# Kernel optimization log

Hardware: AMD Instinct MI355X
Metric: run time of the kernel (lower is better)

The kernel has to match this reference:

```python
import jax, jax.numpy as jnp
import numpy as np

N_NODES = 100000
N_EDGES = 1600000
D_IN = 128
D_H = 128
N_LAYERS = 3
N_OUT = 10
N_GRAPHS = 64


def setup_inputs() -> dict:
    key = jax.random.key(0)
    ks = jax.random.split(key, 12)
    glorot = lambda k, fi, fo: jax.random.normal(k, (fi, fo), jnp.float32) * np.sqrt(2.0 / (fi + fo))
    return {
        "x": jax.random.normal(ks[0], (N_NODES, D_IN), jnp.float32),
        "edge_index": jax.random.randint(ks[1], (2, N_EDGES), 0, N_NODES, jnp.int64 if jax.config.jax_enable_x64 else jnp.int32),
        "batch": jnp.sort(jax.random.randint(ks[2], (N_NODES,), 0, N_GRAPHS)),
        "target_size": N_GRAPHS,
        "W1": glorot(ks[3], D_IN, D_H), "b1": jnp.zeros((D_H,), jnp.float32),
        "W2": glorot(ks[4], D_H, D_H), "b2": jnp.zeros((D_H,), jnp.float32),
        "W3": glorot(ks[5], D_H, D_H), "b3": jnp.zeros((D_H,), jnp.float32),
        "lin1_w": glorot(ks[6], N_LAYERS * D_H, D_H), "lin1_b": jnp.zeros((D_H,), jnp.float32),
        "lin2_w": glorot(ks[7], D_H, N_OUT), "lin2_b": jnp.zeros((N_OUT,), jnp.float32),
    }


def _gcn_conv(x, src, dst, norm, W, b, n_nodes):
    # PyG GCNConv: h = X W; out[dst] += norm * h[src]; out += b
    h = x @ W
    msg = h[src] * norm[:, None]            # [E+N, D_H] gathered messages
    out = jax.ops.segment_sum(msg, dst, num_segments=n_nodes)
    return out + b


def reference(x, edge_index, batch, target_size, W1, b1, W2, b2, W3, b3,
              lin1_w, lin1_b, lin2_w, lin2_b):
    n = x.shape[0]
    loops = jnp.arange(n, dtype=edge_index.dtype)
    src = jnp.concatenate([edge_index[0], loops])   # add self-loops (PyG default)
    dst = jnp.concatenate([edge_index[1], loops])
    deg = jax.ops.segment_sum(jnp.ones_like(src, dtype=x.dtype), dst, num_segments=n)
    dinv = jnp.where(deg > 0, jax.lax.rsqrt(deg), 0.0)
    norm = dinv[src] * dinv[dst]                    # symmetric normalization

    h1 = jax.nn.relu(_gcn_conv(x, src, dst, norm, W1, b1, n))
    h2 = jax.nn.relu(_gcn_conv(h1, src, dst, norm, W2, b2, n))
    h3 = jax.nn.relu(_gcn_conv(h2, src, dst, norm, W3, b3, n))
    h = jnp.concatenate([h1, h2, h3], axis=-1)      # JumpingKnowledge 'cat' -> [N, 3*D_H]

    # global_mean_pool over graphs
    counts = jax.ops.segment_sum(jnp.ones((n,), x.dtype), batch, num_segments=target_size)
    pooled = jax.ops.segment_sum(h, batch, num_segments=target_size)
    pooled = pooled / jnp.maximum(counts, 1.0)[:, None]

    g = jax.nn.relu(pooled @ lin1_w + lin1_b)       # dropout is identity at inference
    logits = g @ lin2_w + lin2_b
    return jax.nn.log_softmax(logits, axis=-1)
```

## Files before the change

kernel.cpp:

```cpp
#include <hip/hip_runtime.h>

#define NN 100000
#define NE 1600000
#define DH 128
#define NG 64

#define NBUCKU 98
#define EPB 4096
#define NBLK_BIN 391
#define CAP 20480

#define LDH 136

typedef __attribute__((ext_vector_type(2))) _Float16 half2v;
typedef __attribute__((ext_vector_type(4))) _Float16 half4;
typedef __attribute__((ext_vector_type(8))) _Float16 half8;
typedef __attribute__((ext_vector_type(4))) float f32x4;

__device__ inline unsigned int enc8(_Float16 h) {
  unsigned short b = __builtin_bit_cast(unsigned short, h);
  unsigned short r = (unsigned short)(b + 0x7F + ((b >> 8) & 1));
  return (unsigned int)(r >> 8);
}
__device__ inline half2v d02(unsigned int u) {
  return __builtin_bit_cast(half2v, (u << 8) & 0xFF00FF00u);
}
__device__ inline half2v d13(unsigned int u) {
  return __builtin_bit_cast(half2v, u & 0xFF00FF00u);
}


__global__ __launch_bounds__(256) void k_build(const int* __restrict__ esrc,
                                               const int* __restrict__ edst,
                                               const int* __restrict__ batch,
                                               const float* __restrict__ W0,
                                               const float* __restrict__ W1,
                                               const float* __restrict__ W2,
                                               int* __restrict__ bucketCursor,
                                               unsigned int* __restrict__ pairs,
                                               int* __restrict__ startg,
                                               _Float16* __restrict__ Wt) {
  int b = blockIdx.x, t = threadIdx.x;
  int gtid = b * 256 + t;

  if (gtid < 3 * DH * DH) {
    int l = gtid >> 14;
    int rem = gtid & 16383;
    int n = rem >> 7, k = rem & 127;
    const float* W = (l == 0) ? W0 : (l == 1) ? W1 : W2;
    Wt[(size_t)l * DH * DH + n * DH + k] = (_Float16)W[k * DH + n];
  }
  if (gtid < NN) {
    int bat = batch[gtid];
    int prev = (gtid == 0) ? -1 : batch[gtid - 1];
    for (int g = prev + 1; g <= bat; ++g) startg[g] = gtid;
    if (gtid == NN - 1)
      for (int g = bat + 1; g <= NG; ++g) startg[g] = NN;
  }

  __shared__ int h[NBUCKU];
  __shared__ int cur[NBUCKU];
  if (t < NBUCKU) h[t] = 0;
  __syncthreads();
  int base = b * EPB;
#pragma unroll
  for (int i = 0; i < EPB / 256; ++i) {
    int e = base + i * 256 + t;
    if (e < NE) atomicAdd(&h[edst[e] >> 10], 1);
  }
  __syncthreads();
  if (t < NBUCKU) {
    int rel = atomicAdd(&bucketCursor[t], h[t]);
    cur[t] = t * CAP + rel;
  }
  __syncthreads();
#pragma unroll
  for (int i = 0; i < EPB / 256; ++i) {
    int e = base + i * 256 + t;
    if (e < NE) {
      int d = edst[e];
      int q = atomicAdd(&cur[d >> 10], 1);
      pairs[q] = ((unsigned int)esrc[e] << 10) | (unsigned int)(d & 1023);
    }
  }
}


__global__ __launch_bounds__(256) void k_finalize(const unsigned int* __restrict__ pairs,
                                                  const int* __restrict__ bucketCursor,
                                                  int* __restrict__ offA,
                                                  int* __restrict__ offB,
                                                  float* __restrict__ dinv,
                                                  int* __restrict__ csr_src) {
  __shared__ int cnt[1024];
  __shared__ int tsum[256];
  int b = blockIdx.x, t = threadIdx.x;
  int nodeBase = b << 10;
  for (int i = t; i < 1024; i += 256) cnt[i] = 0;
  __syncthreads();
  int pStart = b * CAP;
  int pEnd = pStart + bucketCursor[b];
  for (int p = pStart + t; p < pEnd; p += 256)
    atomicAdd(&cnt[pairs[p] & 1023], 1);
  __syncthreads();
  int c0 = cnt[t * 4], c1 = cnt[t * 4 + 1], c2 = cnt[t * 4 + 2], c3 = cnt[t * 4 + 3];
  tsum[t] = c0 + c1 + c2 + c3;
  __syncthreads();
  for (int off = 1; off < 256; off <<= 1) {
    int v = (t >= off) ? tsum[t - off] : 0;
    __syncthreads();
    tsum[t] += v;
    __syncthreads();
  }
  int basep = pStart + ((t > 0) ? tsum[t - 1] : 0);
  int e0 = basep, e1 = basep + c0, e2 = e1 + c1, e3 = e2 + c2;
  __syncthreads();
  cnt[t * 4] = e0; cnt[t * 4 + 1] = e1; cnt[t * 4 + 2] = e2; cnt[t * 4 + 3] = e3;
  int g = nodeBase + t * 4;
  if (g < NN)     { offA[g] = e0;     offB[g] = e1;      dinv[g] = rsqrtf((float)c0 + 1.f); }
  if (g + 1 < NN) { offA[g + 1] = e1; offB[g + 1] = e2;  dinv[g + 1] = rsqrtf((float)c1 + 1.f); }
  if (g + 2 < NN) { offA[g + 2] = e2; offB[g + 2] = e3;  dinv[g + 2] = rsqrtf((float)c2 + 1.f); }
  if (g + 3 < NN) { offA[g + 3] = e3; offB[g + 3] = e3 + c3; dinv[g + 3] = rsqrtf((float)c3 + 1.f); }
  __syncthreads();
  for (int p = pStart + t; p < pEnd; p += 256) {
    unsigned int pr = pairs[p];
    int pos = atomicAdd(&cnt[pr & 1023], 1);
    csr_src[pos] = (int)(pr >> 10);
  }
}


template <bool F32IN>
__global__ __launch_bounds__(256) void k_gemm(const void* __restrict__ Ap,
                                              const _Float16* __restrict__ Wt,
                                              const float* __restrict__ dinv,
                                              unsigned char* __restrict__ Out8) {
  __shared__ _Float16 Wl[128 * LDH];
  int tid = threadIdx.x;
  int rowBase = blockIdx.x * 128;

#pragma unroll
  for (int i = 0; i < 8; ++i) {
    int chunk = tid + i * 256;
    int r = chunk >> 4, c = (chunk & 15) * 8;
    *(half8*)&Wl[r * LDH + c] = *(const half8*)(Wt + r * DH + c);
  }

  int wv = tid >> 6;
  int lane = tid & 63;
  int n16 = lane & 15;
  int quad = lane >> 4;

  int r0 = rowBase + wv * 32 + n16;
  int r1 = r0 + 16;

  half8 af[2][4];
  if (F32IN) {
    const float* A = (const float*)Ap;
#pragma unroll
    for (int kk = 0; kk < 4; ++kk) {
      half8 z = {};
      if (r0 < NN) {
        float4 lo = *(const float4*)(A + (size_t)r0 * DH + quad * 8 + kk * 32);
        float4 hi = *(const float4*)(A + (size_t)r0 * DH + quad * 8 + kk * 32 + 4);
        z = (half8){(_Float16)lo.x, (_Float16)lo.y, (_Float16)lo.z, (_Float16)lo.w,
                    (_Float16)hi.x, (_Float16)hi.y, (_Float16)hi.z, (_Float16)hi.w};
      }
      af[0][kk] = z;
      half8 z1 = {};
      if (r1 < NN) {
        float4 lo = *(const float4*)(A + (size_t)r1 * DH + quad * 8 + kk * 32);
        float4 hi = *(const float4*)(A + (size_t)r1 * DH + quad * 8 + kk * 32 + 4);
        z1 = (half8){(_Float16)lo.x, (_Float16)lo.y, (_Float16)lo.z, (_Float16)lo.w,
                     (_Float16)hi.x, (_Float16)hi.y, (_Float16)hi.z, (_Float16)hi.w};
      }
      af[1][kk] = z1;
    }
  } else {
    const _Float16* A = (const _Float16*)Ap;
#pragma unroll
    for (int kk = 0; kk < 4; ++kk) {
      half8 z = {};
      if (r0 < NN) z = *(const half8*)(A + (size_t)r0 * DH + quad * 8 + kk * 32);
      af[0][kk] = z;
      half8 z1 = {};
      if (r1 < NN) z1 = *(const half8*)(A + (size_t)r1 * DH + quad * 8 + kk * 32);
      af[1][kk] = z1;
    }
  }
  __syncthreads();

  f32x4 acc[2][8];
#pragma unroll
  for (int mt = 0; mt < 2; ++mt)
#pragma unroll
    for (int ct = 0; ct < 8; ++ct) acc[mt][ct] = (f32x4){0.f, 0.f, 0.f, 0.f};

  const _Float16* bp = &Wl[n16 * LDH + quad * 8];
#pragma unroll
  for (int kk = 0; kk < 4; ++kk) {
#pragma unroll
    for (int ct = 0; ct < 8; ++ct) {
      half8 bf = *(const half8*)(bp + (size_t)ct * 16 * LDH + kk * 32);
      acc[0][ct] = __builtin_amdgcn_mfma_f32_16x16x32_f16(af[0][kk], bf, acc[0][ct], 0, 0, 0);
      acc[1][ct] = __builtin_amdgcn_mfma_f32_16x16x32_f16(af[1][kk], bf, acc[1][ct], 0, 0, 0);
    }
  }

  float dv[2][4];
#pragma unroll
  for (int mt = 0; mt < 2; ++mt)
#pragma unroll
    for (int r = 0; r < 4; ++r) {
      int gr = rowBase + wv * 32 + mt * 16 + quad * 4 + r;
      dv[mt][r] = (gr < NN) ? dinv[gr] : 0.f;
    }

  __syncthreads();
#pragma unroll
  for (int mt = 0; mt < 2; ++mt)
#pragma unroll
    for (int ct = 0; ct < 8; ++ct)
#pragma unroll
      for (int r = 0; r < 4; ++r)
        Wl[(wv * 32 + mt * 16 + quad * 4 + r) * LDH + ct * 16 + n16] =
            (_Float16)(acc[mt][ct][r] * dv[mt][r]);
  __syncthreads();

#pragma unroll
  for (int i = 0; i < 8; ++i) {
    int chunk = tid + i * 256;
    int r = chunk >> 4, c = (chunk & 15) * 8;
    int gr = rowBase + r;
    if (gr < NN) {
      half8 v = *(const half8*)&Wl[r * LDH + c];
      unsigned int lo = enc8(v[0]) | (enc8(v[1]) << 8) | (enc8(v[2]) << 16) | (enc8(v[3]) << 24);
      unsigned int hi = enc8(v[4]) | (enc8(v[5]) << 8) | (enc8(v[6]) << 16) | (enc8(v[7]) << 24);
      uint2 st = {lo, hi};
      *(uint2*)(Out8 + (size_t)gr * DH + c) = st;
    }
  }
}


__global__ __launch_bounds__(512) void k_fused(const unsigned char* __restrict__ hs8_in,
                                               const int* __restrict__ csr_src,
                                               const int* __restrict__ offA,
                                               const int* __restrict__ offB,
                                               const float* __restrict__ dinv,
                                               const float* __restrict__ bias,
                                               const int* __restrict__ batch,
                                               const int* __restrict__ startg,
                                               float* __restrict__ pooled,
                                               int colOff,
                                               const _Float16* __restrict__ Wt,
                                               unsigned char* __restrict__ hs8_out) {
  __shared__ _Float16 Hl[64 * LDH];
  __shared__ _Float16 Wl[128 * LDH];
  int tid = threadIdx.x;
  int n0 = blockIdx.x * 64;

#pragma unroll
  for (int i = 0; i < 4; ++i) {
    int chunk = tid + i * 512;
    int r = chunk >> 4, c = (chunk & 15) * 8;
    *(half8*)&Wl[r * LDH + c] = *(const half8*)(Wt + r * DH + c);
  }

  int nd = tid >> 3;
  int part = tid & 7;
  int n = n0 + nd;
  bool valid = (n < NN);

  half2v acc[8];
#pragma unroll
  for (int i = 0; i < 8; ++i) acc[i] = (half2v){(_Float16)0, (_Float16)0};

  if (valid) {
    const unsigned char* bp = hs8_in + part * 16;
    uint4 us = *(const uint4*)(bp + (size_t)n * DH);
    acc[0] += d02(us.x); acc[1] += d13(us.x);
    acc[2] += d02(us.y); acc[3] += d13(us.y);
    acc[4] += d02(us.z); acc[5] += d13(us.z);
    acc[6] += d02(us.w); acc[7] += d13(us.w);
    int s = offA[n], e = offB[n];
    int p = s;
    for (; p + 3 < e; p += 4) {
      int s0 = csr_src[p], s1 = csr_src[p + 1], s2 = csr_src[p + 2], s3 = csr_src[p + 3];
      uint4 u0 = *(const uint4*)(bp + (size_t)s0 * DH);
      uint4 u1 = *(const uint4*)(bp + (size_t)s1 * DH);
      uint4 u2 = *(const uint4*)(bp + (size_t)s2 * DH);
      uint4 u3 = *(const uint4*)(bp + (size_t)s3 * DH);
      acc[0] += d02(u0.x); acc[1] += d13(u0.x); acc[2] += d02(u0.y); acc[3] += d13(u0.y);
      acc[4] += d02(u0.z); acc[5] += d13(u0.z); acc[6] += d02(u0.w); acc[7] += d13(u0.w);
      acc[0] += d02(u1.x); acc[1] += d13(u1.x); acc[2] += d02(u1.y); acc[3] += d13(u1.y);
      acc[4] += d02(u1.z); acc[5] += d13(u1.z); acc[6] += d02(u1.w); acc[7] += d13(u1.w);
      acc[0] += d02(u2.x); acc[1] += d13(u2.x); acc[2] += d02(u2.y); acc[3] += d13(u2.y);
      acc[4] += d02(u2.z); acc[5] += d13(u2.z); acc[6] += d02(u2.w); acc[7] += d13(u2.w);
      acc[0] += d02(u3.x); acc[1] += d13(u3.x); acc[2] += d02(u3.y); acc[3] += d13(u3.y);
      acc[4] += d02(u3.z); acc[5] += d13(u3.z); acc[6] += d02(u3.w); acc[7] += d13(u3.w);
    }
    for (; p < e; ++p) {
      int s0 = csr_src[p];
      uint4 u0 = *(const uint4*)(bp + (size_t)s0 * DH);
      acc[0] += d02(u0.x); acc[1] += d13(u0.x); acc[2] += d02(u0.y); acc[3] += d13(u0.y);
      acc[4] += d02(u0.z); acc[5] += d13(u0.z); acc[6] += d02(u0.w); acc[7] += d13(u0.w);
    }
  }

  float dv = valid ? dinv[n] : 0.f;
#pragma unroll
  for (int w = 0; w < 4; ++w) {
    int dim = part * 16 + w * 4;
    float4 b4 = *(const float4*)(bias + dim);
    float h0 = valid ? fmaxf(fmaf((float)acc[2 * w][0], dv, b4.x), 0.f) : 0.f;
    float h1 = valid ? fmaxf(fmaf((float)acc[2 * w + 1][0], dv, b4.y), 0.f) : 0.f;
    float h2 = valid ? fmaxf(fmaf((float)acc[2 * w][1], dv, b4.z), 0.f) : 0.f;
    float h3 = valid ? fmaxf(fmaf((float)acc[2 * w + 1][1], dv, b4.w), 0.f) : 0.f;
    half4 hh = {(_Float16)h0, (_Float16)h1, (_Float16)h2, (_Float16)h3};
    *(half4*)&Hl[nd * LDH + dim] = hh;
  }
  __syncthreads();

  if (tid < DH) {
    int nEnd = (n0 + 64 < NN) ? n0 + 64 : NN;
    int gF = batch[n0];
    int gL = batch[nEnd - 1];
    for (int g = gF; g <= gL; ++g) {
      int rs = (startg[g] > n0) ? startg[g] : n0;
      int re = (startg[g + 1] < nEnd) ? startg[g + 1] : nEnd;
      if (re > rs) {
        float sum = 0.f;
        for (int r2 = rs; r2 < re; ++r2) sum += (float)Hl[(r2 - n0) * LDH + tid];
        atomicAdd(&pooled[g * (3 * DH) + colOff + tid], sum);
      }
    }
  }

  int wv = tid >> 6;
  int lane = tid & 63;
  int n16 = lane & 15;
  int quad = lane >> 4;
  int m16 = wv >> 1;
  int ctB = (wv & 1) * 4;

  f32x4 acc2[4];
#pragma unroll
  for (int ct = 0; ct < 4; ++ct) acc2[ct] = (f32x4){0.f, 0.f, 0.f, 0.f};

  const _Float16* ap = &Hl[(m16 * 16 + n16) * LDH + quad * 8];
#pragma unroll
  for (int kk = 0; kk < 4; ++kk) {
    half8 af = *(const half8*)(ap + kk * 32);
#pragma unroll
    for (int ct = 0; ct < 4; ++ct) {
      half8 bf = *(const half8*)&Wl[((ctB + ct) * 16 + n16) * LDH + quad * 8 + kk * 32];
      acc2[ct] = __builtin_amdgcn_mfma_f32_16x16x32_f16(af, bf, acc2[ct], 0, 0, 0);
    }
  }

  float dvo[4];
#pragma unroll
  for (int rr = 0; rr < 4; ++rr) {
    int gr = n0 + m16 * 16 + quad * 4 + rr;
    dvo[rr] = (gr < NN) ? dinv[gr] : 0.f;
  }

  __syncthreads();
#pragma unroll
  for (int ct = 0; ct < 4; ++ct)
#pragma unroll
    for (int rr = 0; rr < 4; ++rr)
      Hl[(m16 * 16 + quad * 4 + rr) * LDH + (ctB + ct) * 16 + n16] =
          (_Float16)(acc2[ct][rr] * dvo[rr]);
  __syncthreads();

#pragma unroll
  for (int i = 0; i < 2; ++i) {
    int chunk = tid + i * 512;
    int r = chunk >> 4, c = (chunk & 15) * 8;
    int gr = n0 + r;
    if (gr < NN) {
      half8 v = *(const half8*)&Hl[r * LDH + c];
      unsigned int lo = enc8(v[0]) | (enc8(v[1]) << 8) | (enc8(v[2]) << 16) | (enc8(v[3]) << 24);
      unsigned int hi = enc8(v[4]) | (enc8(v[5]) << 8) | (enc8(v[6]) << 16) | (enc8(v[7]) << 24);
      uint2 st = {lo, hi};
      *(uint2*)(hs8_out + (size_t)gr * DH + c) = st;
    }
  }
}


__global__ __launch_bounds__(256) void k_aggregate(const unsigned char* __restrict__ hs8,
                                                   const int* __restrict__ csr_src,
                                                   const int* __restrict__ offA,
                                                   const int* __restrict__ offB,
                                                   const float* __restrict__ dinv,
                                                   const float* __restrict__ bias,
                                                   const int* __restrict__ batch,
                                                   float* __restrict__ pooled,
                                                   int colOff) {
  __shared__ float stage[8][DH];
  int tid = threadIdx.x;
  int gid = blockIdx.x * 256 + tid;
  int node = gid >> 5;
  int sub = tid >> 5;
  int lane4 = (gid & 31) * 4;
  int s = offA[node];
  int e = offB[node];

  unsigned int us = *(const unsigned int*)(hs8 + (size_t)node * DH + lane4);
  half2v aE0 = d02(us), aE1 = d13(us);
  half2v aO0 = {(_Float16)0, (_Float16)0}, aO1 = {(_Float16)0, (_Float16)0};

  int p = s;
  for (; p + 3 < e; p += 4) {
    int s0 = csr_src[p];
    int s1 = csr_src[p + 1];
    int s2 = csr_src[p + 2];
    int s3 = csr_src[p + 3];
    unsigned int u0 = *(const unsigned int*)(hs8 + (size_t)s0 * DH + lane4);
    unsigned int u1 = *(const unsigned int*)(hs8 + (size_t)s1 * DH + lane4);
    unsigned int u2 = *(const unsigned int*)(hs8 + (size_t)s2 * DH + lane4);
    unsigned int u3 = *(const unsigned int*)(hs8 + (size_t)s3 * DH + lane4);
    aE0 += d02(u0); aE1 += d13(u0);
    aO0 += d02(u1); aO1 += d13(u1);
    aE0 += d02(u2); aE1 += d13(u2);
    aO0 += d02(u3); aO1 += d13(u3);
  }
  for (; p < e; ++p) {
    int s0 = csr_src[p];
    unsigned int u0 = *(const unsigned int*)(hs8 + (size_t)s0 * DH + lane4);
    aE0 += d02(u0); aE1 += d13(u0);
  }

  float ax = (float)aE0[0] + (float)aO0[0];
  float ay = (float)aE1[0] + (float)aO1[0];
  float az = (float)aE0[1] + (float)aO0[1];
  float aw = (float)aE1[1] + (float)aO1[1];

  float dv = dinv[node];
  float4 b4 = *(const float4*)(bias + lane4);
  float4 r;
  r.x = fmaxf(fmaf(ax, dv, b4.x), 0.f);
  r.y = fmaxf(fmaf(ay, dv, b4.y), 0.f);
  r.z = fmaxf(fmaf(az, dv, b4.z), 0.f);
  r.w = fmaxf(fmaf(aw, dv, b4.w), 0.f);

  int nodeFirst = blockIdx.x * 8;
  int gFirst = batch[nodeFirst];
  int gLast = batch[nodeFirst + 7];
  if (gFirst == gLast) {
    *(float4*)&stage[sub][lane4] = r;
    __syncthreads();
    if (tid < DH) {
      float ssum = 0.f;
#pragma unroll
      for (int w = 0; w < 8; ++w) ssum += stage[w][tid];
      atomicAdd(&pooled[gFirst * (3 * DH) + colOff + tid], ssum);
    }
  } else {
    int g = batch[node];
    float* pp = &pooled[g * (3 * DH) + colOff + lane4];
    atomicAdd(pp + 0, r.x);
    atomicAdd(pp + 1, r.y);
    atomicAdd(pp + 2, r.z);
    atomicAdd(pp + 3, r.w);
  }
}


__global__ __launch_bounds__(128) void k_head(const float* __restrict__ pooled,
                                              const int* __restrict__ startg,
                                              const float* __restrict__ l1w,
                                              const float* __restrict__ l1b,
                                              const float* __restrict__ l2w,
                                              const float* __restrict__ l2b,
                                              float* __restrict__ out) {
  __shared__ float pr[3 * DH];
  __shared__ float grow[DH];
  __shared__ float lg[16];
  int g = blockIdx.x, t = threadIdx.x;
  float cnt = (float)(startg[g + 1] - startg[g]);
  float inv = 1.0f / fmaxf(cnt, 1.0f);
  for (int k = t; k < 3 * DH; k += 128) pr[k] = pooled[g * (3 * DH) + k] * inv;
  __syncthreads();
  float acc = l1b[t];
  for (int k = 0; k < 3 * DH; ++k) acc = fmaf(pr[k], l1w[k * DH + t], acc);
  grow[t] = fmaxf(acc, 0.f);
  __syncthreads();
  if (t < 10) {
    float a = l2b[t];
    for (int k = 0; k < DH; ++k) a = fmaf(grow[k], l2w[k * 10 + t], a);
    lg[t] = a;
  }
  __syncthreads();
  if (t < 10) {
    float m = lg[0];
    for (int i = 1; i < 10; ++i) m = fmaxf(m, lg[i]);
    float sum = 0.f;
    for (int i = 0; i < 10; ++i) sum += expf(lg[i] - m);
    out[g * 10 + t] = lg[t] - m - logf(sum);
  }
}


extern "C" void kernel_launch(void* const* d_in, const int* in_sizes, int n_in,
                              void* d_out, int out_size, void* d_ws, size_t ws_size,
                              hipStream_t stream) {
  const float* x = (const float*)d_in[0];
  const int* ei = (const int*)d_in[1];
  const int* esrc = ei;
  const int* edst = ei + NE;
  const int* batch = (const int*)d_in[2];
  const float* W0 = (const float*)d_in[4];
  const float* W1 = (const float*)d_in[6];
  const float* W2 = (const float*)d_in[8];
  const float* B[3] = {(const float*)d_in[5], (const float*)d_in[7], (const float*)d_in[9]};
  const float* l1w = (const float*)d_in[10];
  const float* l1b = (const float*)d_in[11];
  const float* l2w = (const float*)d_in[12];
  const float* l2b = (const float*)d_in[13];
  float* out = (float*)d_out;

  char* ws = (char*)d_ws;
  size_t off = 0;
  auto alloc = [&](size_t bytes) {
    char* p = ws + off;
    off = (off + bytes + 255) & ~(size_t)255;
    return p;
  };
  float* pooled = (float*)alloc((size_t)NG * 3 * DH * 4);
  int* bucketCursor = (int*)alloc(NBUCKU * 4);
  size_t msBytes = (size_t)NG * 3 * DH * 4 + 512;

  int* offA = (int*)alloc((size_t)NN * 4);
  int* offB = (int*)alloc((size_t)NN * 4);
  float* dinv = (float*)alloc((size_t)NN * 4);
  int* startg = (int*)alloc((NG + 1) * 4);
  _Float16* Wt = (_Float16*)alloc((size_t)3 * DH * DH * 2);
  unsigned char* hs8A = (unsigned char*)alloc((size_t)NN * DH);
  unsigned char* hs8B = (unsigned char*)alloc((size_t)NN * DH);
  unsigned int* pairs = (unsigned int*)alloc((size_t)NBUCKU * CAP * 4);
  int* csr_src = (int*)alloc((size_t)NBUCKU * CAP * 4);

  hipMemsetAsync(pooled, 0, msBytes, stream);

  k_build<<<NBLK_BIN, 256, 0, stream>>>(esrc, edst, batch, W0, W1, W2,
                                        bucketCursor, pairs, startg, Wt);
  k_finalize<<<NBUCKU, 256, 0, stream>>>(pairs, bucketCursor, offA, offB, dinv, csr_src);

  k_gemm<true><<<(NN + 127) / 128, 256, 0, stream>>>((const void*)x, Wt, dinv, hs8A);

  int nFusedBlk = (NN + 63) / 64;
  k_fused<<<nFusedBlk, 512, 0, stream>>>(hs8A, csr_src, offA, offB, dinv, B[0], batch,
                                         startg, pooled, 0,
                                         Wt + (size_t)1 * DH * DH, hs8B);
  k_fused<<<nFusedBlk, 512, 0, stream>>>(hs8B, csr_src, offA, offB, dinv, B[1], batch,
                                         startg, pooled, DH,
                                         Wt + (size_t)2 * DH * DH, hs8A);

  k_aggregate<<<(NN * 32) / 256, 256, 0, stream>>>(hs8A, csr_src, offA, offB, dinv, B[2],
                                                   batch, pooled, 2 * DH);

  k_head<<<NG, 128, 0, stream>>>(pooled, startg, l1w, l1b, l2w, l2b, out);
}
```

Baseline: 369.5 us.

## Split fp8 feature rows into two column halves to shrink gather working set

Stores the 8-bit encoded node features as two planes of 64 columns each and makes the aggregation kernels gather one half at a time. Each pass then touches a 6.4 MB table instead of 12.8 MB, so the randomly gathered rows are more likely to stay in cache. The cost is walking each CSR neighbour list twice, with narrower loads per thread. The pooled zeroing also moves out of a separate memset into k_build, and the final aggregate kernel remaps threads to 16 per node.

```diff
diff --git a/kernel.cpp b/kernel.cpp
--- a/kernel.cpp
+++ b/kernel.cpp
@@ -11,6 +11,7 @@
 #define CAP 20480
 
 #define LDH 136
+#define HHALF ((size_t)NN * 64)
 
 typedef __attribute__((ext_vector_type(2))) _Float16 half2v;
 typedef __attribute__((ext_vector_type(4))) _Float16 half4;
@@ -39,10 +40,12 @@
                                                int* __restrict__ bucketCursor,
                                                unsigned int* __restrict__ pairs,
                                                int* __restrict__ startg,
+                                               float* __restrict__ pooled,
                                                _Float16* __restrict__ Wt) {
   int b = blockIdx.x, t = threadIdx.x;
   int gtid = b * 256 + t;
 
+  if (gtid < NG * 3 * DH) pooled[gtid] = 0.f;
   if (gtid < 3 * DH * DH) {
     int l = gtid >> 14;
     int rem = gtid & 16383;
@@ -237,7 +240,9 @@
       unsigned int lo = enc8(v[0]) | (enc8(v[1]) << 8) | (enc8(v[2]) << 16) | (enc8(v[3]) << 24);
       unsigned int hi = enc8(v[4]) | (enc8(v[5]) << 8) | (enc8(v[6]) << 16) | (enc8(v[7]) << 24);
       uint2 st = {lo, hi};
-      *(uint2*)(Out8 + (size_t)gr * DH + c) = st;
+      unsigned char* dst = (c < 64) ? (Out8 + (size_t)gr * 64 + c)
+                                    : (Out8 + HHALF + (size_t)gr * 64 + (c - 64));
+      *(uint2*)dst = st;
     }
   }
 }
@@ -268,57 +273,52 @@
   }
 
   int nd = tid >> 3;
-  int part = tid & 7;
+  int prt = tid & 7;
   int n = n0 + nd;
   bool valid = (n < NN);
-
-  half2v acc[8];
-#pragma unroll
-  for (int i = 0; i < 8; ++i) acc[i] = (half2v){(_Float16)0, (_Float16)0};
-
-  if (valid) {
-    const unsigned char* bp = hs8_in + part * 16;
-    uint4 us = *(const uint4*)(bp + (size_t)n * DH);
-    acc[0] += d02(us.x); acc[1] += d13(us.x);
-    acc[2] += d02(us.y); acc[3] += d13(us.y);
-    acc[4] += d02(us.z); acc[5] += d13(us.z);
-    acc[6] += d02(us.w); acc[7] += d13(us.w);
-    int s = offA[n], e = offB[n];
-    int p = s;
-    for (; p + 3 < e; p += 4) {
-      int s0 = csr_src[p], s1 = csr_src[p + 1], s2 = csr_src[p + 2], s3 = csr_src[p + 3];
-      uint4 u0 = *(const uint4*)(bp + (size_t)s0 * DH);
-      uint4 u1 = *(const uint4*)(bp + (size_t)s1 * DH);
-      uint4 u2 = *(const uint4*)(bp + (size_t)s2 * DH);
-      uint4 u3 = *(const uint4*)(bp + (size_t)s3 * DH);
-      acc[0] += d02(u0.x); acc[1] += d13(u0.x); acc[2] += d02(u0.y); acc[3] += d13(u0.y);
-      acc[4] += d02(u0.z); acc[5] += d13(u0.z); acc[6] += d02(u0.w); acc[7] += d13(u0.w);
-      acc[0] += d02(u1.x); acc[1] += d13(u1.x); acc[2] += d02(u1.y); acc[3] += d13(u1.y);
-      acc[4] += d02(u1.z); acc[5] += d13(u1.z); acc[6] += d02(u1.w); acc[7] += d13(u1.w);
-      acc[0] += d02(u2.x); acc[1] += d13(u2.x); acc[2] += d02(u2.y); acc[3] += d13(u2.y);
-      acc[4] += d02(u2.z); acc[5] += d13(u2.z); acc[6] += d02(u2.w); acc[7] += d13(u2.w);
-      acc[0] += d02(u3.x); acc[1] += d13(u3.x); acc[2] += d02(u3.y); acc[3] += d13(u3.y);
-      acc[4] += d02(u3.z); acc[5] += d13(u3.z); acc[6] += d02(u3.w); acc[7] += d13(u3.w);
-    }
-    for (; p < e; ++p) {
-      int s0 = csr_src[p];
-      uint4 u0 = *(const uint4*)(bp + (size_t)s0 * DH);
-      acc[0] += d02(u0.x); acc[1] += d13(u0.x); acc[2] += d02(u0.y); acc[3] += d13(u0.y);
-      acc[4] += d02(u0.z); acc[5] += d13(u0.z); acc[6] += d02(u0.w); acc[7] += d13(u0.w);
-    }
-  }
-
-  float dv = valid ? dinv[n] : 0.f;
-#pragma unroll
-  for (int w = 0; w < 4; ++w) {
-    int dim = part * 16 + w * 4;
-    float4 b4 = *(const float4*)(bias + dim);
-    float h0 = valid ? fmaxf(fmaf((float)acc[2 * w][0], dv, b4.x), 0.f) : 0.f;
-    float h1 = valid ? fmaxf(fmaf((float)acc[2 * w + 1][0], dv, b4.y), 0.f) : 0.f;
-    float h2 = valid ? fmaxf(fmaf((float)acc[2 * w][1], dv, b4.z), 0.f) : 0.f;
-    float h3 = valid ? fmaxf(fmaf((float)acc[2 * w + 1][1], dv, b4.w), 0.f) : 0.f;
-    half4 hh = {(_Float16)h0, (_Float16)h1, (_Float16)h2, (_Float16)h3};
-    *(half4*)&Hl[nd * LDH + dim] = hh;
+  int s = 0, e = 0;
+  float dv = 0.f;
+  if (valid) { s = offA[n]; e = offB[n]; dv = dinv[n]; }
+
+#pragma unroll
+  for (int h = 0; h < 2; ++h) {
+    half2v a0 = {(_Float16)0, (_Float16)0}, a1 = a0, a2 = a0, a3 = a0;
+    if (valid) {
+      const unsigned char* rb = hs8_in + (size_t)h * HHALF + prt * 8;
+      uint2 us = *(const uint2*)(rb + (size_t)n * 64);
+      a0 += d02(us.x); a1 += d13(us.x); a2 += d02(us.y); a3 += d13(us.y);
+      int p = s;
+      for (; p + 3 < e; p += 4) {
+        int s0 = csr_src[p], s1 = csr_src[p + 1], s2 = csr_src[p + 2], s3 = csr_src[p + 3];
+        uint2 u0 = *(const uint2*)(rb + (size_t)s0 * 64);
+        uint2 u1 = *(const uint2*)(rb + (size_t)s1 * 64);
+        uint2 u2 = *(const uint2*)(rb + (size_t)s2 * 64);
+        uint2 u3 = *(const uint2*)(rb + (size_t)s3 * 64);
+        a0 += d02(u0.x); a1 += d13(u0.x); a2 += d02(u0.y); a3 += d13(u0.y);
+        a0 += d02(u1.x); a1 += d13(u1.x); a2 += d02(u1.y); a3 += d13(u1.y);
+        a0 += d02(u2.x); a1 += d13(u2.x); a2 += d02(u2.y); a3 += d13(u2.y);
+        a0 += d02(u3.x); a1 += d13(u3.x); a2 += d02(u3.y); a3 += d13(u3.y);
+      }
+      for (; p < e; ++p) {
+        int s0 = csr_src[p];
+        uint2 u0 = *(const uint2*)(rb + (size_t)s0 * 64);
+        a0 += d02(u0.x); a1 += d13(u0.x); a2 += d02(u0.y); a3 += d13(u0.y);
+      }
+    }
+    int dim = h * 64 + prt * 8;
+    float4 bA = *(const float4*)(bias + dim);
+    float4 bB = *(const float4*)(bias + dim + 4);
+    float h0 = valid ? fmaxf(fmaf((float)a0[0], dv, bA.x), 0.f) : 0.f;
+    float h1 = valid ? fmaxf(fmaf((float)a1[0], dv, bA.y), 0.f) : 0.f;
+    float h2 = valid ? fmaxf(fmaf((float)a0[1], dv, bA.z), 0.f) : 0.f;
+    float h3 = valid ? fmaxf(fmaf((float)a1[1], dv, bA.w), 0.f) : 0.f;
+    float h4 = valid ? fmaxf(fmaf((float)a2[0], dv, bB.x), 0.f) : 0.f;
+    float h5 = valid ? fmaxf(fmaf((float)a3[0], dv, bB.y), 0.f) : 0.f;
+    float h6 = valid ? fmaxf(fmaf((float)a2[1], dv, bB.z), 0.f) : 0.f;
+    float h7 = valid ? fmaxf(fmaf((float)a3[1], dv, bB.w), 0.f) : 0.f;
+    half8 hh = {(_Float16)h0, (_Float16)h1, (_Float16)h2, (_Float16)h3,
+                (_Float16)h4, (_Float16)h5, (_Float16)h6, (_Float16)h7};
+    *(half8*)&Hl[nd * LDH + dim] = hh;
   }
   __syncthreads();
 
@@ -385,7 +385,9 @@
       unsigned int lo = enc8(v[0]) | (enc8(v[1]) << 8) | (enc8(v[2]) << 16) | (enc8(v[3]) << 24);
       unsigned int hi = enc8(v[4]) | (enc8(v[5]) << 8) | (enc8(v[6]) << 16) | (enc8(v[7]) << 24);
       uint2 st = {lo, hi};
-      *(uint2*)(hs8_out + (size_t)gr * DH + c) = st;
+      unsigned char* dst = (c < 64) ? (hs8_out + (size_t)gr * 64 + c)
+                                    : (hs8_out + HHALF + (size_t)gr * 64 + (c - 64));
+      *(uint2*)dst = st;
     }
   }
 }
@@ -400,72 +402,75 @@
                                                    const int* __restrict__ batch,
                                                    float* __restrict__ pooled,
                                                    int colOff) {
-  __shared__ float stage[8][DH];
+  __shared__ float stage[16][DH];
   int tid = threadIdx.x;
   int gid = blockIdx.x * 256 + tid;
-  int node = gid >> 5;
-  int sub = tid >> 5;
-  int lane4 = (gid & 31) * 4;
+  int node = gid >> 4;
+  int sub = tid >> 4;
+  int prt = gid & 15;
   int s = offA[node];
   int e = offB[node];
-
-  unsigned int us = *(const unsigned int*)(hs8 + (size_t)node * DH + lane4);
-  half2v aE0 = d02(us), aE1 = d13(us);
-  half2v aO0 = {(_Float16)0, (_Float16)0}, aO1 = {(_Float16)0, (_Float16)0};
-
-  int p = s;
-  for (; p + 3 < e; p += 4) {
-    int s0 = csr_src[p];
-    int s1 = csr_src[p + 1];
-    int s2 = csr_src[p + 2];
-    int s3 = csr_src[p + 3];
-    unsigned int u0 = *(const unsigned int*)(hs8 + (size_t)s0 * DH + lane4);
-    unsigned int u1 = *(const unsigned int*)(hs8 + (size_t)s1 * DH + lane4);
-    unsigned int u2 = *(const unsigned int*)(hs8 + (size_t)s2 * DH + lane4);
-    unsigned int u3 = *(const unsigned int*)(hs8 + (size_t)s3 * DH + lane4);
-    aE0 += d02(u0); aE1 += d13(u0);
-    aO0 += d02(u1); aO1 += d13(u1);
-    aE0 += d02(u2); aE1 += d13(u2);
-    aO0 += d02(u3); aO1 += d13(u3);
-  }
-  for (; p < e; ++p) {
-    int s0 = csr_src[p];
-    unsigned int u0 = *(const unsigned int*)(hs8 + (size_t)s0 * DH + lane4);
-    aE0 += d02(u0); aE1 += d13(u0);
-  }
-
-  float ax = (float)aE0[0] + (float)aO0[0];
-  float ay = (float)aE1[0] + (float)aO1[0];
-  float az = (float)aE0[1] + (float)aO0[1];
-  float aw = (float)aE1[1] + (float)aO1[1];
-
   float dv = dinv[node];
-  float4 b4 = *(const float4*)(bias + lane4);
-  float4 r;
-  r.x = fmaxf(fmaf(ax, dv, b4.x), 0.f);
-  r.y = fmaxf(fmaf(ay, dv, b4.y), 0.f);
-  r.z = fmaxf(fmaf(az, dv, b4.z), 0.f);
-  r.w = fmaxf(fmaf(aw, dv, b4.w), 0.f);
-
-  int nodeFirst = blockIdx.x * 8;
+
+  float res[2][4];
+#pragma unroll
+  for (int h = 0; h < 2; ++h) {
+    const unsigned char* rb = hs8 + (size_t)h * HHALF + prt * 4;
+    unsigned int us = *(const unsigned int*)(rb + (size_t)node * 64);
+    half2v aE0 = d02(us), aE1 = d13(us);
+    half2v aO0 = {(_Float16)0, (_Float16)0}, aO1 = {(_Float16)0, (_Float16)0};
+    int p = s;
+    for (; p + 3 < e; p += 4) {
+      int s0 = csr_src[p];
+      int s1 = csr_src[p + 1];
+      int s2 = csr_src[p + 2];
+      int s3 = csr_src[p + 3];
+      unsigned int u0 = *(const unsigned int*)(rb + (size_t)s0 * 64);
+      unsigned int u1 = *(const unsigned int*)(rb + (size_t)s1 * 64);
+      unsigned int u2 = *(const unsigned int*)(rb + (size_t)s2 * 64);
+      unsigned int u3 = *(const unsigned int*)(rb + (size_t)s3 * 64);
+      aE0 += d02(u0); aE1 += d13(u0);
+      aO0 += d02(u1); aO1 += d13(u1);
+      aE0 += d02(u2); aE1 += d13(u2);
+      aO0 += d02(u3); aO1 += d13(u3);
+    }
+    for (; p < e; ++p) {
+      int s0 = csr_src[p];
+      unsigned int u0 = *(const unsigned int*)(rb + (size_t)s0 * 64);
+      aE0 += d02(u0); aE1 += d13(u0);
+    }
+    float ax = (float)aE0[0] + (float)aO0[0];
+    float ay = (float)aE1[0] + (float)aO1[0];
+    float az = (float)aE0[1] + (float)aO0[1];
+    float aw = (float)aE1[1] + (float)aO1[1];
+    float4 b4 = *(const float4*)(bias + h * 64 + prt * 4);
+    res[h][0] = fmaxf(fmaf(ax, dv, b4.x), 0.f);
+    res[h][1] = fmaxf(fmaf(ay, dv, b4.y), 0.f);
+    res[h][2] = fmaxf(fmaf(az, dv, b4.z), 0.f);
+    res[h][3] = fmaxf(fmaf(aw, dv, b4.w), 0.f);
+  }
+
+  int nodeFirst = blockIdx.x * 16;
   int gFirst = batch[nodeFirst];
-  int gLast = batch[nodeFirst + 7];
+  int gLast = batch[nodeFirst + 15];
   if (gFirst == gLast) {
-    *(float4*)&stage[sub][lane4] = r;
+    *(float4*)&stage[sub][prt * 4] = make_float4(res[0][0], res[0][1], res[0][2], res[0][3]);
+    *(float4*)&stage[sub][64 + prt * 4] = make_float4(res[1][0], res[1][1], res[1][2], res[1][3]);
     __syncthreads();
     if (tid < DH) {
       float ssum = 0.f;
 #pragma unroll
-      for (int w = 0; w < 8; ++w) ssum += stage[w][tid];
+      for (int w = 0; w < 16; ++w) ssum += stage[w][tid];
       atomicAdd(&pooled[gFirst * (3 * DH) + colOff + tid], ssum);
     }
   } else {
     int g = batch[node];
-    float* pp = &pooled[g * (3 * DH) + colOff + lane4];
-    atomicAdd(pp + 0, r.x);
-    atomicAdd(pp + 1, r.y);
-    atomicAdd(pp + 2, r.z);
-    atomicAdd(pp + 3, r.w);
+    float* pp = &pooled[g * (3 * DH) + colOff];
+#pragma unroll
+    for (int j = 0; j < 4; ++j) {
+      atomicAdd(pp + prt * 4 + j, res[0][j]);
+      atomicAdd(pp + 64 + prt * 4 + j, res[1][j]);
+    }
   }
 }
 
@@ -530,10 +535,8 @@
     off = (off + bytes + 255) & ~(size_t)255;
     return p;
   };
+  int* bucketCursor = (int*)alloc(NBUCKU * 4);
   float* pooled = (float*)alloc((size_t)NG * 3 * DH * 4);
-  int* bucketCursor = (int*)alloc(NBUCKU * 4);
-  size_t msBytes = (size_t)NG * 3 * DH * 4 + 512;
-
   int* offA = (int*)alloc((size_t)NN * 4);
   int* offB = (int*)alloc((size_t)NN * 4);
   float* dinv = (float*)alloc((size_t)NN * 4);
@@ -544,10 +547,10 @@
   unsigned int* pairs = (unsigned int*)alloc((size_t)NBUCKU * CAP * 4);
   int* csr_src = (int*)alloc((size_t)NBUCKU * CAP * 4);
 
-  hipMemsetAsync(pooled, 0, msBytes, stream);
+  hipMemsetAsync(bucketCursor, 0, 512, stream);
 
   k_build<<<NBLK_BIN, 256, 0, stream>>>(esrc, edst, batch, W0, W1, W2,
-                                        bucketCursor, pairs, startg, Wt);
+                                        bucketCursor, pairs, startg, pooled, Wt);
   k_finalize<<<NBUCKU, 256, 0, stream>>>(pairs, bucketCursor, offA, offB, dinv, csr_src);
 
   k_gemm<true><<<(NN + 127) / 128, 256, 0, stream>>>((const void*)x, Wt, dinv, hs8A);
@@ -560,8 +563,8 @@
                                          startg, pooled, DH,
                                          Wt + (size_t)2 * DH * DH, hs8A);
 
-  k_aggregate<<<(NN * 32) / 256, 256, 0, stream>>>(hs8A, csr_src, offA, offB, dinv, B[2],
-                                                   batch, pooled, 2 * DH);
+  k_aggregate<<<(NN + 15) / 16, 256, 0, stream>>>(hs8A, csr_src, offA, offB, dinv, B[2],
+                                                  batch, pooled, 2 * DH);
 
   k_head<<<NG, 128, 0, stream>>>(pooled, startg, l1w, l1b, l2w, l2b, out);
 }
```

Result: slower. 398.1 us (+7.7%).
